# Kernel optimization log

Hardware: AMD Instinct MI355X
Metric: run time of the kernel (lower is better)

Reference implementation:

```python
import jax, jax.numpy as jnp
import numpy as np

B, N, D = 262144, 3, 64

def setup_inputs() -> dict:
    key = jax.random.key(0)
    k = jax.random.split(key, 6)
    lim1 = 1.0 / np.sqrt(2 * D)
    lim2 = 1.0 / np.sqrt(D)
    nodes = jax.random.normal(k[0], (B, N, D), dtype=jnp.float32)
    W1 = jax.random.uniform(k[1], (2 * D, D), jnp.float32, -lim1, lim1)
    b1 = jax.random.uniform(k[2], (D,), jnp.float32, -lim1, lim1)
    W2 = jax.random.uniform(k[3], (D, D), jnp.float32, -lim2, lim2)
    b2 = jax.random.uniform(k[4], (D,), jnp.float32, -lim2, lim2)
    edge_attn = jnp.array([[0.0, 1.5, 0.5], [1.5, 0.0, 0.8], [0.3, 0.8, 0.0]], dtype=jnp.float32)
    return {"nodes": nodes, "W1": W1, "b1": b1, "W2": W2, "b2": b2, "edge_attn": edge_attn}

def reference(nodes, W1, b1, W2, b2, edge_attn):
    b, n, d = nodes.shape
    # pairwise concat: (B, N, N, 2D) with ni varying over axis 1, nj over axis 2
    ni = jnp.broadcast_to(nodes[:, :, None, :], (b, n, n, d))
    nj = jnp.broadcast_to(nodes[:, None, :, :], (b, n, n, d))
    x = jnp.concatenate([ni, nj], axis=-1)            # (B,N,N,2D)
    h = jax.nn.gelu(x @ W1 + b1, approximate=False)   # torch nn.GELU default = exact erf
    msg = h @ W2 + b2                                 # (B,N,N,D)
    attn = jax.nn.softmax(edge_attn, axis=-1)         # (N,N)
    agg = jnp.einsum('ij,bijd->bid', attn, msg)       # weighted sum over j
    return agg
```

## Files before the change

### kernel.cpp

```cpp
#include <hip/hip_runtime.h>
#include <hip/hip_bf16.h>
#include <math.h>

typedef __attribute__((ext_vector_type(8))) short bf16x8;
typedef __attribute__((ext_vector_type(4))) float f32x4;

#define WSTR 68
#define OSTR 80

__device__ __forceinline__ short f2bs(float f) {
    union { __hip_bfloat16 b; short s; } u;
    u.b = __float2bfloat16(f);
    return u.s;
}

__device__ __forceinline__ unsigned short f2b_int(float f) {
    union { float f; unsigned int u; } x; x.f = f;
    unsigned int r = x.u + 0x7FFFu + ((x.u >> 16) & 1u);
    return (unsigned short)(r >> 16);
}

__device__ __forceinline__ float gelu_t(float x) {
    float x2 = x * x;
    float z  = x * fmaf(0.10294324f, x2, 2.3022082f);
    float e  = __builtin_amdgcn_exp2f(z);
    float r  = __builtin_amdgcn_rcpf(1.0f + e);
    return fmaf(x, -r, x);
}

__global__ void prep_k(const float* __restrict__ W1, const float* __restrict__ W2,
                       const float* __restrict__ ea, unsigned short* __restrict__ w1t,
                       unsigned short* __restrict__ w2t, float* __restrict__ attn)
{
    int gid = blockIdx.x * 256 + threadIdx.x;
    if (gid < 128 * 64) {
        int n = gid >> 6, k = gid & 63;
        float v = (n < 64) ? W1[k * 64 + n] : W1[(64 + k) * 64 + (n - 64)];
        w1t[gid] = f2b_int(v);
    } else if (gid < 12288) {
        int idx = gid - 8192;
        int n = idx >> 6, k = idx & 63;
        w2t[idx] = f2b_int(W2[k * 64 + n]);
    }
    if (gid < 9) {
        int i = gid / 3, j = gid % 3;
        float e0 = ea[i*3+0], e1 = ea[i*3+1], e2 = ea[i*3+2];
        float mx = fmaxf(e0, fmaxf(e1, e2));
        float d = expf(e0-mx) + expf(e1-mx) + expf(e2-mx);
        attn[gid] = expf(ea[i*3+j] - mx) / d;
    }
}

__global__ __launch_bounds__(256, 3)
void edge_mfma18(const float* __restrict__ nodes,
                 const unsigned short* __restrict__ w1t,
                 const unsigned short* __restrict__ w2t,
                 const float* __restrict__ attn9,
                 const float* __restrict__ b1,
                 const float* __restrict__ b2,
                 float* __restrict__ out)
{
    __shared__ __align__(16) unsigned short Ws[8192];
    __shared__ __align__(16) float Un[4 * 12 * OSTR];

    const int t = threadIdx.x;
    const int lane = t & 63, wave = t >> 6;
    const int q = lane >> 4, r16 = lane & 15;
    float*          Ow = Un + wave * 12 * OSTR;
    unsigned short* Gw = (unsigned short*)Ow;

    {
        const ulonglong2* src = (const ulonglong2*)w1t;
        ulonglong2* dst = (ulonglong2*)Ws;
        #pragma unroll
        for (int i = 0; i < 4; ++i) {
            int c = t + i * 256;
            int n = c >> 3, k8 = c & 7;
            dst[(c & ~7) | (k8 ^ (n & 7))] = src[c];
        }
    }

    const int bA = r16 >> 2;
    const int iA = r16 & 3;
    const int iAr = (iA == 3) ? 0 : iA;

    const int sxor = (r16 & 7) << 3;
    const unsigned short* w1b0 = Ws + r16 * 64 + ((q * 8) ^ sxor);
    const unsigned short* w1b1 = Ws + r16 * 64 + ((32 + q * 8) ^ sxor);
    unsigned short*       gww  = Gw + (q * 4) * WSTR + r16;
    const unsigned short* gfrb = Gw + r16 * WSTR + q * 8;
    float*                oww  = Ow + (q * 3) * OSTR + r16;
    const float*          owr  = Ow + q * OSTR + r16 * 4;

    bf16x8 w2f[4][2];
    #pragma unroll
    for (int nt = 0; nt < 4; ++nt)
        #pragma unroll
        for (int ks = 0; ks < 2; ++ks)
            w2f[nt][ks] = *(const bf16x8*)&w2t[(nt*16 + r16) * 64 + ks*32 + q*8];

    float aw[9];
    #pragma unroll
    for (int i = 0; i < 9; ++i) {
        union { float f; int u; } c; c.f = attn9[i];
        c.u = __builtin_amdgcn_readfirstlane(c.u);
        aw[i] = c.f;
    }
    float b1c[4], b2c[4];
    #pragma unroll
    for (int nt = 0; nt < 4; ++nt) { b1c[nt] = b1[nt*16 + r16]; b2c[nt] = b2[nt*16 + r16]; }

    const int batch0 = blockIdx.x * 64 + wave * 16;

    const float* xptr = nodes + ((long)(batch0 + bA)) * 192 + iAr * 64 + q * 8;
    float*       optr = out + (long)batch0 * 192 + lane * 4;

    __syncthreads();

    #pragma unroll
    for (int mt = 0; mt < 4; ++mt) {
        f32x4 x0 = *(const f32x4*)(xptr);
        f32x4 x1 = *(const f32x4*)(xptr + 4);
        f32x4 x2v = *(const f32x4*)(xptr + 32);
        f32x4 x3 = *(const f32x4*)(xptr + 36);
        bf16x8 afr0, afr1;
        #pragma unroll
        for (int e = 0; e < 4; ++e) {
            afr0[e]   = f2bs(x0[e]);  afr0[4+e] = f2bs(x1[e]);
            afr1[e]   = f2bs(x2v[e]); afr1[4+e] = f2bs(x3[e]);
        }

        #pragma unroll
        for (int nt = 0; nt < 4; ++nt) {
            f32x4 z = {0.f, 0.f, 0.f, 0.f};
            z = __builtin_amdgcn_mfma_f32_16x16x32_bf16(afr0, *(const bf16x8*)(w1b0 + nt*1024), z, 0, 0, 0);
            z = __builtin_amdgcn_mfma_f32_16x16x32_bf16(afr1, *(const bf16x8*)(w1b1 + nt*1024), z, 0, 0, 0);
            f32x4 y = {0.f, 0.f, 0.f, 0.f};
            y = __builtin_amdgcn_mfma_f32_16x16x32_bf16(afr0, *(const bf16x8*)(w1b0 + 4096 + nt*1024), y, 0, 0, 0);
            y = __builtin_amdgcn_mfma_f32_16x16x32_bf16(afr1, *(const bf16x8*)(w1b1 + 4096 + nt*1024), y, 0, 0, 0);

            float u0 = z[0] + b1c[nt], u1 = z[1] + b1c[nt], u2 = z[2] + b1c[nt];
            float gg0 = 0.f, gg1 = 0.f, gg2 = 0.f;
            #pragma unroll
            for (int j = 0; j < 3; ++j) {
                float vj = y[j];
                float gl0 = gelu_t(u0 + vj);
                float gl1 = gelu_t(u1 + vj);
                float gl2 = gelu_t(u2 + vj);
                gg0 = fmaf(aw[0*3+j], gl0, gg0);
                gg1 = fmaf(aw[1*3+j], gl1, gg1);
                gg2 = fmaf(aw[2*3+j], gl2, gg2);
            }
            gww[0 * WSTR + nt*16] = (unsigned short)f2bs(gg0);
            gww[1 * WSTR + nt*16] = (unsigned short)f2bs(gg1);
            gww[2 * WSTR + nt*16] = (unsigned short)f2bs(gg2);
        }

        bf16x8 gfr0 = *(const bf16x8*)(gfrb);
        bf16x8 gfr1 = *(const bf16x8*)(gfrb + 32);
        #pragma unroll
        for (int nt = 0; nt < 4; ++nt) {
            f32x4 acc = {0.f, 0.f, 0.f, 0.f};
            acc = __builtin_amdgcn_mfma_f32_16x16x32_bf16(gfr0, w2f[nt][0], acc, 0, 0, 0);
            acc = __builtin_amdgcn_mfma_f32_16x16x32_bf16(gfr1, w2f[nt][1], acc, 0, 0, 0);
            #pragma unroll
            for (int r = 0; r < 3; ++r)
                oww[r * OSTR + nt*16] = acc[r] + b2c[nt];
        }

        #pragma unroll
        for (int s = 0; s < 3; ++s) {
            f32x4 v = *(const f32x4*)(owr + 4 * s * OSTR);
            __builtin_nontemporal_store(v, (f32x4*)(optr + 256 * s));
        }

        xptr += 768;
        optr += 768;
    }
}

extern "C" void kernel_launch(void* const* d_in, const int* in_sizes, int n_in,
                              void* d_out, int out_size, void* d_ws, size_t ws_size,
                              hipStream_t stream)
{
    const float* nodes = (const float*)d_in[0];
    const float* W1    = (const float*)d_in[1];
    const float* b1    = (const float*)d_in[2];
    const float* W2    = (const float*)d_in[3];
    const float* b2    = (const float*)d_in[4];
    const float* ea    = (const float*)d_in[5];
    float* out = (float*)d_out;

    unsigned short* w1t = (unsigned short*)d_ws;
    unsigned short* w2t = w1t + 8192;
    float* attn = (float*)(w2t + 4096);

    prep_k<<<48, 256, 0, stream>>>(W1, W2, ea, w1t, w2t, attn);

    const int groups = (out_size / 64) / 3 / 64;
    edge_mfma18<<<groups, 256, 0, stream>>>(nodes, w1t, w2t, attn, b1, b2, out);
}
```

Measured before the change: 81.88 us.

## Process two batch tiles per pass to reuse W1 fragments from LDS

Each pass of the main loop now handles two 16-batch m-tiles instead of one. The W1 B-fragments are read from shared memory once per n-tile and fed to the MFMAs of both tiles, which halves those shared-memory reads. Each wave gets two GELU staging buffers so the two tiles' hidden activations do not overwrite each other. The cost is more registers held live, in a kernel already bounded at three blocks per CU, and a larger shared-memory footprint per block.

```diff
diff --git a/kernel.cpp b/kernel.cpp
--- a/kernel.cpp
+++ b/kernel.cpp
@@ -52,7 +52,7 @@
 }
 
 __global__ __launch_bounds__(256, 3)
-void edge_mfma18(const float* __restrict__ nodes,
+void edge_mfma19(const float* __restrict__ nodes,
                  const unsigned short* __restrict__ w1t,
                  const unsigned short* __restrict__ w2t,
                  const float* __restrict__ attn9,
@@ -61,13 +61,15 @@
                  float* __restrict__ out)
 {
     __shared__ __align__(16) unsigned short Ws[8192];
-    __shared__ __align__(16) float Un[4 * 12 * OSTR];
+    __shared__ __align__(16) float Un[4 * 1536];
 
     const int t = threadIdx.x;
     const int lane = t & 63, wave = t >> 6;
     const int q = lane >> 4, r16 = lane & 15;
-    float*          Ow = Un + wave * 12 * OSTR;
-    unsigned short* Gw = (unsigned short*)Ow;
+    float*          wb  = Un + wave * 1536;
+    unsigned short* G0  = (unsigned short*)wb;
+    unsigned short* G1  = (unsigned short*)(wb + 960);
+    float*          Ow  = wb;
 
     {
         const ulonglong2* src = (const ulonglong2*)w1t;
@@ -87,10 +89,10 @@
     const int sxor = (r16 & 7) << 3;
     const unsigned short* w1b0 = Ws + r16 * 64 + ((q * 8) ^ sxor);
     const unsigned short* w1b1 = Ws + r16 * 64 + ((32 + q * 8) ^ sxor);
-    unsigned short*       gww  = Gw + (q * 4) * WSTR + r16;
-    const unsigned short* gfrb = Gw + r16 * WSTR + q * 8;
-    float*                oww  = Ow + (q * 3) * OSTR + r16;
-    const float*          owr  = Ow + q * OSTR + r16 * 4;
+    const int gwoff = (q * 4) * WSTR + r16;
+    const int groff = r16 * WSTR + q * 8;
+    float*       oww = Ow + (q * 3) * OSTR + r16;
+    const float* owr = Ow + q * OSTR + r16 * 4;
 
     bf16x8 w2f[4][2];
     #pragma unroll
@@ -111,71 +113,83 @@
     for (int nt = 0; nt < 4; ++nt) { b1c[nt] = b1[nt*16 + r16]; b2c[nt] = b2[nt*16 + r16]; }
 
     const int batch0 = blockIdx.x * 64 + wave * 16;
-
     const float* xptr = nodes + ((long)(batch0 + bA)) * 192 + iAr * 64 + q * 8;
     float*       optr = out + (long)batch0 * 192 + lane * 4;
 
     __syncthreads();
 
     #pragma unroll
-    for (int mt = 0; mt < 4; ++mt) {
-        f32x4 x0 = *(const f32x4*)(xptr);
-        f32x4 x1 = *(const f32x4*)(xptr + 4);
-        f32x4 x2v = *(const f32x4*)(xptr + 32);
-        f32x4 x3 = *(const f32x4*)(xptr + 36);
-        bf16x8 afr0, afr1;
-        #pragma unroll
-        for (int e = 0; e < 4; ++e) {
-            afr0[e]   = f2bs(x0[e]);  afr0[4+e] = f2bs(x1[e]);
-            afr1[e]   = f2bs(x2v[e]); afr1[4+e] = f2bs(x3[e]);
+    for (int p = 0; p < 2; ++p) {
+        bf16x8 afr[2][2];
+        #pragma unroll
+        for (int m2 = 0; m2 < 2; ++m2) {
+            const float* xp = xptr + (p*2 + m2) * 768;
+            f32x4 x0 = *(const f32x4*)(xp);
+            f32x4 x1 = *(const f32x4*)(xp + 4);
+            f32x4 x2v = *(const f32x4*)(xp + 32);
+            f32x4 x3 = *(const f32x4*)(xp + 36);
+            #pragma unroll
+            for (int e = 0; e < 4; ++e) {
+                afr[m2][0][e]   = f2bs(x0[e]);  afr[m2][0][4+e] = f2bs(x1[e]);
+                afr[m2][1][e]   = f2bs(x2v[e]); afr[m2][1][4+e] = f2bs(x3[e]);
+            }
         }
 
         #pragma unroll
         for (int nt = 0; nt < 4; ++nt) {
-            f32x4 z = {0.f, 0.f, 0.f, 0.f};
-            z = __builtin_amdgcn_mfma_f32_16x16x32_bf16(afr0, *(const bf16x8*)(w1b0 + nt*1024), z, 0, 0, 0);
-            z = __builtin_amdgcn_mfma_f32_16x16x32_bf16(afr1, *(const bf16x8*)(w1b1 + nt*1024), z, 0, 0, 0);
-            f32x4 y = {0.f, 0.f, 0.f, 0.f};
-            y = __builtin_amdgcn_mfma_f32_16x16x32_bf16(afr0, *(const bf16x8*)(w1b0 + 4096 + nt*1024), y, 0, 0, 0);
-            y = __builtin_amdgcn_mfma_f32_16x16x32_bf16(afr1, *(const bf16x8*)(w1b1 + 4096 + nt*1024), y, 0, 0, 0);
-
-            float u0 = z[0] + b1c[nt], u1 = z[1] + b1c[nt], u2 = z[2] + b1c[nt];
-            float gg0 = 0.f, gg1 = 0.f, gg2 = 0.f;
-            #pragma unroll
-            for (int j = 0; j < 3; ++j) {
-                float vj = y[j];
-                float gl0 = gelu_t(u0 + vj);
-                float gl1 = gelu_t(u1 + vj);
-                float gl2 = gelu_t(u2 + vj);
-                gg0 = fmaf(aw[0*3+j], gl0, gg0);
-                gg1 = fmaf(aw[1*3+j], gl1, gg1);
-                gg2 = fmaf(aw[2*3+j], gl2, gg2);
-            }
-            gww[0 * WSTR + nt*16] = (unsigned short)f2bs(gg0);
-            gww[1 * WSTR + nt*16] = (unsigned short)f2bs(gg1);
-            gww[2 * WSTR + nt*16] = (unsigned short)f2bs(gg2);
-        }
-
-        bf16x8 gfr0 = *(const bf16x8*)(gfrb);
-        bf16x8 gfr1 = *(const bf16x8*)(gfrb + 32);
-        #pragma unroll
-        for (int nt = 0; nt < 4; ++nt) {
-            f32x4 acc = {0.f, 0.f, 0.f, 0.f};
-            acc = __builtin_amdgcn_mfma_f32_16x16x32_bf16(gfr0, w2f[nt][0], acc, 0, 0, 0);
-            acc = __builtin_amdgcn_mfma_f32_16x16x32_bf16(gfr1, w2f[nt][1], acc, 0, 0, 0);
-            #pragma unroll
-            for (int r = 0; r < 3; ++r)
-                oww[r * OSTR + nt*16] = acc[r] + b2c[nt];
-        }
-
-        #pragma unroll
-        for (int s = 0; s < 3; ++s) {
-            f32x4 v = *(const f32x4*)(owr + 4 * s * OSTR);
-            __builtin_nontemporal_store(v, (f32x4*)(optr + 256 * s));
-        }
-
-        xptr += 768;
-        optr += 768;
+            bf16x8 fu0 = *(const bf16x8*)(w1b0 + nt*1024);
+            bf16x8 fu1 = *(const bf16x8*)(w1b1 + nt*1024);
+            bf16x8 fv0 = *(const bf16x8*)(w1b0 + 4096 + nt*1024);
+            bf16x8 fv1 = *(const bf16x8*)(w1b1 + 4096 + nt*1024);
+            #pragma unroll
+            for (int m2 = 0; m2 < 2; ++m2) {
+                f32x4 z = {0.f, 0.f, 0.f, 0.f};
+                z = __builtin_amdgcn_mfma_f32_16x16x32_bf16(afr[m2][0], fu0, z, 0, 0, 0);
+                z = __builtin_amdgcn_mfma_f32_16x16x32_bf16(afr[m2][1], fu1, z, 0, 0, 0);
+                f32x4 y = {0.f, 0.f, 0.f, 0.f};
+                y = __builtin_amdgcn_mfma_f32_16x16x32_bf16(afr[m2][0], fv0, y, 0, 0, 0);
+                y = __builtin_amdgcn_mfma_f32_16x16x32_bf16(afr[m2][1], fv1, y, 0, 0, 0);
+
+                float u0 = z[0] + b1c[nt], u1 = z[1] + b1c[nt], u2 = z[2] + b1c[nt];
+                float gg0 = 0.f, gg1 = 0.f, gg2 = 0.f;
+                #pragma unroll
+                for (int j = 0; j < 3; ++j) {
+                    float vj = y[j];
+                    float gl0 = gelu_t(u0 + vj);
+                    float gl1 = gelu_t(u1 + vj);
+                    float gl2 = gelu_t(u2 + vj);
+                    gg0 = fmaf(aw[0*3+j], gl0, gg0);
+                    gg1 = fmaf(aw[1*3+j], gl1, gg1);
+                    gg2 = fmaf(aw[2*3+j], gl2, gg2);
+                }
+                unsigned short* Gm = (m2 == 0) ? G0 : G1;
+                Gm[gwoff + 0*WSTR + nt*16] = (unsigned short)f2bs(gg0);
+                Gm[gwoff + 1*WSTR + nt*16] = (unsigned short)f2bs(gg1);
+                Gm[gwoff + 2*WSTR + nt*16] = (unsigned short)f2bs(gg2);
+            }
+        }
+
+        #pragma unroll
+        for (int m2 = 0; m2 < 2; ++m2) {
+            const unsigned short* Gm = (m2 == 0) ? G0 : G1;
+            bf16x8 gfr0 = *(const bf16x8*)(Gm + groff);
+            bf16x8 gfr1 = *(const bf16x8*)(Gm + groff + 32);
+            #pragma unroll
+            for (int nt = 0; nt < 4; ++nt) {
+                f32x4 acc = {0.f, 0.f, 0.f, 0.f};
+                acc = __builtin_amdgcn_mfma_f32_16x16x32_bf16(gfr0, w2f[nt][0], acc, 0, 0, 0);
+                acc = __builtin_amdgcn_mfma_f32_16x16x32_bf16(gfr1, w2f[nt][1], acc, 0, 0, 0);
+                #pragma unroll
+                for (int r = 0; r < 3; ++r)
+                    oww[r * OSTR + nt*16] = acc[r] + b2c[nt];
+            }
+            float* ob = optr + (p*2 + m2) * 768;
+            #pragma unroll
+            for (int s = 0; s < 3; ++s) {
+                f32x4 v = *(const f32x4*)(owr + 4 * s * OSTR);
+                __builtin_nontemporal_store(v, (f32x4*)(ob + 256 * s));
+            }
+        }
     }
 }
 
@@ -198,5 +212,5 @@
     prep_k<<<48, 256, 0, stream>>>(W1, W2, ea, w1t, w2t, attn);
 
     const int groups = (out_size / 64) / 3 / 64;
-    edge_mfma18<<<groups, 256, 0, stream>>>(nodes, w1t, w2t, attn, b1, b2, out);
-}
+    edge_mfma19<<<groups, 256, 0, stream>>>(nodes, w1t, w2t, attn, b1, b2, out);
+}
```

After: 81.05 us. No clear change (-1.0%).
